# Kernel optimization log

Hardware: AMD Instinct MI355X
Metric: run time of the kernel (lower is better)

The kernel has to match this reference:

```python
import jax, jax.numpy as jnp
import numpy as np

D, DFF, H = 1024, 4096, 16
B, S, L = 4, 4096, 512


def setup_inputs() -> dict:
    key = jax.random.key(0)
    ks = jax.random.split(key, 16)
    w = lambda k, shape: (jax.random.normal(k, shape, jnp.float32) * 0.02)
    return {
        "x": jax.random.normal(ks[0], (B, S, D), jnp.float32),
        "limited_time_offer": jax.random.normal(ks[1], (B, L, D), jnp.float32),
        "src_src_self_mask": jnp.ones((B, 1, 1, S), bool),
        "lto_src_cross_mask": jnp.ones((B, 1, 1, S), bool),
        "sa_wq": w(ks[2], (D, D)), "sa_wk": w(ks[3], (D, D)),
        "sa_wv": w(ks[4], (D, D)), "sa_wo": w(ks[5], (D, D)),
        "ca_wq": w(ks[6], (D, D)), "ca_wk": w(ks[7], (D, D)),
        "ca_wv": w(ks[8], (D, D)), "ca_wo": w(ks[9], (D, D)),
        "ff_w1": w(ks[10], (D, DFF)), "ff_b1": jnp.zeros((DFF,), jnp.float32),
        "ff_w2": w(ks[11], (DFF, D)), "ff_b2": jnp.zeros((D,), jnp.float32),
        "ln1_a": jnp.ones((D,), jnp.float32), "ln1_b": jnp.zeros((D,), jnp.float32),
        "ln2_a": jnp.ones((D,), jnp.float32), "ln2_b": jnp.zeros((D,), jnp.float32),
        "ln3_a": jnp.ones((D,), jnp.float32), "ln3_b": jnp.zeros((D,), jnp.float32),
    }


def _ln(x, alpha, bias, eps=1e-6):
    # torch: (x - mean) / (std + eps), std is UNBIASED (ddof=1)
    mean = x.mean(axis=-1, keepdims=True)
    std = jnp.sqrt(x.var(axis=-1, ddof=1, keepdims=True))
    return alpha * (x - mean) / (std + eps) + bias


def _mha_linear(q_in, k_in, v_in, wq, wk, wv, wo):
    Bq, Nq, d = q_in.shape
    dk = d // H
    def proj(t, w):
        t = t @ w  # [b, n, d]
        return t.reshape(t.shape[0], t.shape[1], H, dk).transpose(0, 2, 1, 3)  # bhnd
    Q = jax.nn.relu(proj(q_in, wq)) + 1e-6
    K = jax.nn.relu(proj(k_in, wk)) + 1e-6
    V = proj(v_in, wv)
    kv = jnp.einsum('bhnd,bhne->bhde', K, V)          # KV outer-product state
    qk = jnp.einsum('bhnd,bhde->bhne', Q, kv)         # [b, h, nq, dk]
    # faithful to torch einsum('bhnd,bhne->bhn', Q, K.sum(2, keepdim)):
    # broadcasts n and sums d and e independently
    norm = 1.0 / (Q.sum(-1) * K.sum((2, 3))[:, :, None] + 1e-6)  # [b, h, nq]
    out = (qk * norm[..., None]).transpose(0, 2, 1, 3).reshape(Bq, Nq, d)
    return out @ wo


def reference(x, limited_time_offer, src_src_self_mask, lto_src_cross_mask,
              sa_wq, sa_wk, sa_wv, sa_wo,
              ca_wq, ca_wk, ca_wv, ca_wo,
              ff_w1, ff_b1, ff_w2, ff_b2,
              ln1_a, ln1_b, ln2_a, ln2_b, ln3_a, ln3_b):
    # residual 0: self attention on x
    xn = _ln(x, ln1_a, ln1_b)
    x = x + _mha_linear(xn, xn, xn, sa_wq, sa_wk, sa_wv, sa_wo)
    # residual 1: cross attention, queries = normed lto, keys/values = updated x
    lton = _ln(limited_time_offer, ln2_a, ln2_b)
    lto = limited_time_offer + _mha_linear(lton, x, x, ca_wq, ca_wk, ca_wv, ca_wo)
    # residual 2: feed forward
    fn = _ln(lto, ln3_a, ln3_b)
    ff = jax.nn.relu(fn @ ff_w1 + ff_b1) @ ff_w2 + ff_b2
    return lto + ff
```

## Files before the change

kernel.cpp:

```cpp
#include <hip/hip_runtime.h>
#include <hip/hip_bf16.h>

#define BATCH 4
#define SEQ   4096
#define LSEQ  512
#define DMODEL 1024
#define DFF_  4096
#define NHEAD 16
#define DK_   64
#define NSPLIT 8
#define FFSK  8

typedef __attribute__((ext_vector_type(4))) float f32x4;
typedef __attribute__((ext_vector_type(8))) __bf16 bf16x8;
typedef __attribute__((ext_vector_type(8))) unsigned short ushort8v;
typedef unsigned short u16;

__device__ __forceinline__ u16 f2bf(float f) {
  union { float f; unsigned int u; } c; c.f = f;
  unsigned int u = c.u;
  u += 0x7fffu + ((u >> 16) & 1u);
  return (u16)(u >> 16);
}
__device__ __forceinline__ float bf2f(u16 h) {
  union { unsigned int u; float f; } c; c.u = ((unsigned int)h) << 16;
  return c.f;
}
__device__ __forceinline__ void gload16(const void* g, void* l) {
  __builtin_amdgcn_global_load_lds(
      (const __attribute__((address_space(1))) unsigned int*)g,
      (__attribute__((address_space(3))) unsigned int*)l, 16, 0, 0);
}

__global__ __launch_bounds__(256) void ln_kernel(
    const float* __restrict__ x, const float* __restrict__ alpha,
    const float* __restrict__ beta, u16* __restrict__ y)
{
  const int row = blockIdx.x;
  const int t = threadIdx.x;
  const float4 v = ((const float4*)(x + (size_t)row * DMODEL))[t];
  float s = v.x + v.y + v.z + v.w;
  float ss = v.x * v.x + v.y * v.y + v.z * v.z + v.w * v.w;
  for (int off = 32; off >= 1; off >>= 1) {
    s += __shfl_xor(s, off);
    ss += __shfl_xor(ss, off);
  }
  __shared__ float sbuf[4], ssbuf[4];
  int w = t >> 6;
  if ((t & 63) == 0) { sbuf[w] = s; ssbuf[w] = ss; }
  __syncthreads();
  s = sbuf[0] + sbuf[1] + sbuf[2] + sbuf[3];
  ss = ssbuf[0] + ssbuf[1] + ssbuf[2] + ssbuf[3];
  float mean = s * (1.f / DMODEL);
  float var = (ss - mean * mean * DMODEL) * (1.f / (DMODEL - 1));
  var = fmaxf(var, 0.f);
  float inv = 1.f / (sqrtf(var) + 1e-6f);
  const float4 a = ((const float4*)alpha)[t];
  const float4 bb = ((const float4*)beta)[t];
  ushort4 o;
  o.x = f2bf(a.x * (v.x - mean) * inv + bb.x);
  o.y = f2bf(a.y * (v.y - mean) * inv + bb.y);
  o.z = f2bf(a.z * (v.z - mean) * inv + bb.z);
  o.w = f2bf(a.w * (v.w - mean) * inv + bb.w);
  ((ushort4*)(y + (size_t)row * DMODEL))[t] = o;
}

__global__ __launch_bounds__(256) void wconv_t_kernel(
    const float* __restrict__ W, u16* __restrict__ Wt, int K, int N)
{
  __shared__ float tile[32][33];
  const int n0 = blockIdx.x * 32, k0 = blockIdx.y * 32;
  const int t = threadIdx.x;
  const int r = t >> 3, c4 = (t & 7) * 4;
  float4 v = *(const float4*)&W[(size_t)(k0 + r) * N + n0 + c4];
  tile[r][c4 + 0] = v.x; tile[r][c4 + 1] = v.y;
  tile[r][c4 + 2] = v.z; tile[r][c4 + 3] = v.w;
  __syncthreads();
  ushort4 o;
  o.x = f2bf(tile[c4 + 0][r]);
  o.y = f2bf(tile[c4 + 1][r]);
  o.z = f2bf(tile[c4 + 2][r]);
  o.w = f2bf(tile[c4 + 3][r]);
  *(ushort4*)&Wt[(size_t)(n0 + r) * K + k0 + c4] = o;
}

template <int ACT, bool BIAS, bool RESID, bool OUTBF, bool SPLITK>
__global__ __launch_bounds__(512, 2) void gemm256(
    const u16* __restrict__ A, const u16* __restrict__ Bt,
    const float* __restrict__ bias, const float* __restrict__ R,
    void* __restrict__ Cout, int M, int N, int K, int lda, int ldb)
{
  __shared__ u16 sh[2][2][256 * 64];
  const int t = threadIdx.x;
  const int wid = t >> 6, lane = t & 63;
  const int wr = wid >> 2, wc = wid & 3;
  const int fr = lane & 15, fg = lane >> 4;

  if (SPLITK) {
    const int kp = blockIdx.y;
    A += (size_t)kp * K;
    Bt += (size_t)kp * K;
  }

  int bid = blockIdx.x;
  {
    const int nwg = gridDim.x;
    int q = nwg >> 3, rmd = nwg & 7;
    int xcd = bid & 7, idx = bid >> 3;
    bid = (xcd < rmd ? xcd * (q + 1) : rmd * (q + 1) + (xcd - rmd) * q) + idx;
  }
  const int nxb = N >> 8;
  const int m0 = (bid / nxb) * 256, n0 = (bid % nxb) * 256;

  auto stageA = [&](int buf, int h, int kt) {
#pragma unroll
    for (int j = 0; j < 2; ++j) {
      int idx = j * 512 + t;
      int r = idx >> 3;
      int gc = ((idx & 7) * 16) ^ ((r & 7) << 4);
      const char* src = (const char*)(A + (size_t)(m0 + h * 128 + r) * lda + kt * 64) + gc;
      char* dst = (char*)&sh[buf][0][0] + h * 16384 + j * 8192 + wid * 1024;
      gload16(src, dst);
    }
  };
  auto stageB = [&](int buf, int h, int kt) {
#pragma unroll
    for (int j = 0; j < 2; ++j) {
      int idx = j * 512 + t;
      int r = idx >> 3;
      int gc = ((idx & 7) * 16) ^ ((r & 7) << 4);
      const char* src = (const char*)(Bt + (size_t)(n0 + h * 128 + r) * ldb + kt * 64) + gc;
      char* dst = (char*)&sh[buf][1][0] + h * 16384 + j * 8192 + wid * 1024;
      gload16(src, dst);
    }
  };
  auto rdA = [&](int buf, int mi, int kk) -> bf16x8 {
    int r = wr * 128 + mi * 16 + fr;
    int c = (kk * 64 + fg * 16) ^ ((r & 7) << 4);
    return *(const bf16x8*)((const char*)&sh[buf][0][0] + r * 128 + c);
  };
  auto rdB = [&](int buf, int ni, int kk) -> bf16x8 {
    int r = wc * 64 + ni * 16 + fr;
    int c = (kk * 64 + fg * 16) ^ ((r & 7) << 4);
    return *(const bf16x8*)((const char*)&sh[buf][1][0] + r * 128 + c);
  };

  f32x4 acc[8][4] = {};
  bf16x8 bfrag[4][2];

#define PHASE(BUF, Q, STAGE_STMT, VCNT) do {                                          \
    bf16x8 a00 = rdA(BUF, (Q)*2, 0),     a01 = rdA(BUF, (Q)*2, 1);                     \
    bf16x8 a10 = rdA(BUF, (Q)*2 + 1, 0), a11 = rdA(BUF, (Q)*2 + 1, 1);                 \
    if ((Q) == 0) {                                                                    \
      _Pragma("unroll") for (int ni = 0; ni < 4; ++ni) {                               \
        bfrag[ni][0] = rdB(BUF, ni, 0); bfrag[ni][1] = rdB(BUF, ni, 1); } }            \
    STAGE_STMT;                                                                        \
    __builtin_amdgcn_s_barrier();                                                      \
    asm volatile("s_waitcnt lgkmcnt(0)" ::: "memory");                                 \
    __builtin_amdgcn_s_setprio(1);                                                     \
    _Pragma("unroll") for (int ni = 0; ni < 4; ++ni) {                                 \
      acc[(Q)*2][ni]     = __builtin_amdgcn_mfma_f32_16x16x32_bf16(a00, bfrag[ni][0], acc[(Q)*2][ni], 0, 0, 0);     \
      acc[(Q)*2][ni]     = __builtin_amdgcn_mfma_f32_16x16x32_bf16(a01, bfrag[ni][1], acc[(Q)*2][ni], 0, 0, 0);     \
      acc[(Q)*2 + 1][ni] = __builtin_amdgcn_mfma_f32_16x16x32_bf16(a10, bfrag[ni][0], acc[(Q)*2 + 1][ni], 0, 0, 0); \
      acc[(Q)*2 + 1][ni] = __builtin_amdgcn_mfma_f32_16x16x32_bf16(a11, bfrag[ni][1], acc[(Q)*2 + 1][ni], 0, 0, 0); } \
    __builtin_amdgcn_s_setprio(0);                                                     \
    if ((VCNT) == 4) { asm volatile("s_waitcnt vmcnt(4)" ::: "memory"); }              \
    else if ((VCNT) == 0) { asm volatile("s_waitcnt vmcnt(0)" ::: "memory"); }         \
    __builtin_amdgcn_s_barrier();                                                      \
  } while (0)

  stageA(0, 0, 0); stageA(0, 1, 0);
  stageB(0, 0, 0); stageB(0, 1, 0);
  stageB(1, 0, 1); stageB(1, 1, 1);
  asm volatile("s_waitcnt vmcnt(4)" ::: "memory");
  __builtin_amdgcn_s_barrier();

  const int NIT = K >> 7;
  for (int i = 0; i < NIT - 1; ++i) {
    const int t1 = 2 * i + 1, s0 = 2 * i + 2, s1 = 2 * i + 3;
    PHASE(0, 0, stageA(1, 0, t1), -1);
    PHASE(0, 1, stageA(1, 1, t1), -1);
    PHASE(0, 2, stageB(0, 0, s0), -1);
    PHASE(0, 3, stageB(0, 1, s0), 4);
    PHASE(1, 0, stageA(0, 0, s0), -1);
    PHASE(1, 1, stageA(0, 1, s0), -1);
    PHASE(1, 2, stageB(1, 0, s1), -1);
    PHASE(1, 3, stageB(1, 1, s1), 4);
  }
  {
    const int t1 = 2 * (NIT - 1) + 1;
    PHASE(0, 0, stageA(1, 0, t1), -1);
    PHASE(0, 1, stageA(1, 1, t1), -1);
    PHASE(0, 2, ((void)0), -1);
    PHASE(0, 3, ((void)0), 0);
    PHASE(1, 0, ((void)0), -1);
    PHASE(1, 1, ((void)0), -1);
    PHASE(1, 2, ((void)0), -1);
    PHASE(1, 3, ((void)0), -1);
  }
#undef PHASE

  float* Cf = (float*)Cout;
  if (SPLITK) Cf += (size_t)blockIdx.y * M * N;
  u16* Cb = (u16*)Cout;
  const bool segRelu = (ACT == 3) ? ((n0 >> 10) != 1) : false;
#pragma unroll
  for (int mi = 0; mi < 8; ++mi)
#pragma unroll
    for (int ni = 0; ni < 4; ++ni)
#pragma unroll
      for (int r = 0; r < 4; ++r) {
        int row = m0 + wr * 128 + mi * 16 + fg * 4 + r;
        int col = n0 + wc * 64 + ni * 16 + fr;
        float v = acc[mi][ni][r];
        if (BIAS) v += bias[col];
        if (ACT == 1) v = fmaxf(v, 0.f);
        if (ACT == 2) v = fmaxf(v, 0.f) + 1e-6f;
        if (ACT == 3 && segRelu) v = fmaxf(v, 0.f) + 1e-6f;
        if (RESID) v += R[(size_t)row * N + col];
        if (OUTBF) Cb[(size_t)row * N + col] = f2bf(v);
        else       Cf[(size_t)row * N + col] = v;
      }
}

__global__ __launch_bounds__(256) void ffred_kernel(
    const float* __restrict__ part, const float* __restrict__ bias,
    const float* __restrict__ R, float* __restrict__ out)
{
  const int idx = blockIdx.x * 256 + threadIdx.x;
  const int c4 = idx & 255;
  float4 s = ((const float4*)R)[idx];
  const float4 bv = ((const float4*)bias)[c4];
  s.x += bv.x; s.y += bv.y; s.z += bv.z; s.w += bv.w;
#pragma unroll
  for (int p = 0; p < FFSK; ++p) {
    float4 v = ((const float4*)part)[(size_t)p * 524288 + idx];
    s.x += v.x; s.y += v.y; s.z += v.z; s.w += v.w;
  }
  ((float4*)out)[idx] = s;
}

__global__ __launch_bounds__(256) void ffred_h_kernel(
    const float* __restrict__ part, const float* __restrict__ bias,
    u16* __restrict__ outb)
{
  const size_t idx = (size_t)blockIdx.x * 256 + threadIdx.x;
  const int c4 = idx & 1023;
  const float4 bv = ((const float4*)bias)[c4];
  const float4 p0 = ((const float4*)part)[idx];
  const float4 p1 = ((const float4*)part)[idx + 2097152];
  ushort4 o;
  o.x = f2bf(fmaxf(p0.x + p1.x + bv.x, 0.f));
  o.y = f2bf(fmaxf(p0.y + p1.y + bv.y, 0.f));
  o.z = f2bf(fmaxf(p0.z + p1.z + bv.z, 0.f));
  o.w = f2bf(fmaxf(p0.w + p1.w + bv.w, 0.f));
  ((ushort4*)outb)[idx] = o;
}

template <int ACT, bool BIAS, bool RESID, bool OUTBF>
__global__ __launch_bounds__(256) void gemm_bf16(
    const u16* __restrict__ A, const u16* __restrict__ Bt,
    const float* __restrict__ bias, const float* __restrict__ R,
    void* __restrict__ Cout, int M, int N, int K)
{
  __shared__ u16 As[2][128 * 32];
  __shared__ u16 Bs[2][128 * 32];
  const int t = threadIdx.x;
  const int m0 = blockIdx.y * 128, n0 = blockIdx.x * 128;
  const int lane = t & 63, wid = t >> 6;
  const int wm = (wid >> 1) * 64, wn = (wid & 1) * 64;
  const int fr = lane & 15, fg = lane >> 4;

  const int srow = t >> 2;
  const int scol = (t & 3) * 8;
  const u16* aptr = A + (size_t)(m0 + srow) * K + scol;
  const u16* bptr = Bt + (size_t)(n0 + srow) * K + scol;
  const size_t rstep = (size_t)64 * K;

  f32x4 acc[4][4] = {};

  auto stage = [&](int c, int k0) {
    gload16(aptr + k0,         &As[c][wid * 512]);
    gload16(aptr + k0 + rstep, &As[c][2048 + wid * 512]);
    gload16(bptr + k0,         &Bs[c][wid * 512]);
    gload16(bptr + k0 + rstep, &Bs[c][2048 + wid * 512]);
  };
  auto compute = [&](int c) {
    bf16x8 af[4], bfr[4];
#pragma unroll
    for (int mi = 0; mi < 4; ++mi)
      af[mi] = *(const bf16x8*)&As[c][(wm + mi * 16 + fr) * 32 + fg * 8];
#pragma unroll
    for (int ni = 0; ni < 4; ++ni)
      bfr[ni] = *(const bf16x8*)&Bs[c][(wn + ni * 16 + fr) * 32 + fg * 8];
#pragma unroll
    for (int mi = 0; mi < 4; ++mi)
#pragma unroll
      for (int ni = 0; ni < 4; ++ni)
        acc[mi][ni] = __builtin_amdgcn_mfma_f32_16x16x32_bf16(af[mi], bfr[ni], acc[mi][ni], 0, 0, 0);
  };

  const int NT = K >> 5;
  stage(0, 0);
  asm volatile("s_waitcnt vmcnt(0)" ::: "memory");
  __builtin_amdgcn_s_barrier();
  int cur = 0;
  for (int kt = 0; kt < NT - 1; ++kt) {
    stage(cur ^ 1, (kt + 1) * 32);
    compute(cur);
    asm volatile("s_waitcnt vmcnt(0)" ::: "memory");
    __builtin_amdgcn_s_barrier();
    cur ^= 1;
  }
  compute(cur);

  float* Cf = (float*)Cout;
  u16* Cb = (u16*)Cout;
#pragma unroll
  for (int mi = 0; mi < 4; ++mi)
#pragma unroll
    for (int ni = 0; ni < 4; ++ni)
#pragma unroll
      for (int r = 0; r < 4; ++r) {
        int row = m0 + wm + mi * 16 + fg * 4 + r;
        int col = n0 + wn + ni * 16 + fr;
        float v = acc[mi][ni][r];
        if (BIAS) v += bias[col];
        if (ACT == 1) v = fmaxf(v, 0.f);
        if (ACT == 2) v = fmaxf(v, 0.f) + 1e-6f;
        if (RESID) v += R[(size_t)row * N + col];
        if (OUTBF) Cb[(size_t)row * N + col] = f2bf(v);
        else       Cf[(size_t)row * N + col] = v;
      }
}

__global__ __launch_bounds__(256) void kv_mfma_kernel(
    const u16* __restrict__ KV, float* __restrict__ kvpart,
    float* __restrict__ kpart, int Ntok, int ld)
{
  const int h = blockIdx.x, b = blockIdx.y, sp = blockIdx.z;
  const int rows = Ntok / NSPLIT;
  const int nbeg = sp * rows;
  const u16* Kb = KV + ((size_t)b * Ntok + nbeg) * ld + h * DK_;
  const u16* Vb = Kb + 1024;
  __shared__ u16 Kt[64 * 64];
  __shared__ u16 Vt[64 * 64];
  const int t = threadIdx.x;
  const int lane = t & 63, wid = t >> 6;
  const int fr = lane & 15, fg = lane >> 4;
  const int lrow = t >> 2;
  const int lc0 = (t & 3) * 16;

  f32x4 acc[4] = {};
  float kp = 0.f;

  ushort8v ck[2], cv[2];
  {
    const u16* kr = Kb + (size_t)lrow * ld + lc0;
    const u16* vr = Vb + (size_t)lrow * ld + lc0;
    ck[0] = *(const ushort8v*)kr; ck[1] = *(const ushort8v*)(kr + 8);
    cv[0] = *(const ushort8v*)vr; cv[1] = *(const ushort8v*)(vr + 8);
  }
  for (int c = 0; c < rows; c += 64) {
#pragma unroll
    for (int i = 0; i < 2; ++i)
#pragma unroll
      for (int j = 0; j < 8; ++j) kp += bf2f(ck[i][j]);
    __syncthreads();
#pragma unroll
    for (int i = 0; i < 2; ++i)
#pragma unroll
      for (int j = 0; j < 8; ++j) {
        int d = lc0 + i * 8 + j;
        int byteoff = (d * 128 + lrow * 2) ^ ((d & 7) << 4);
        *(u16*)((char*)Kt + byteoff) = ck[i][j];
        *(u16*)((char*)Vt + byteoff) = cv[i][j];
      }
    __syncthreads();
    if (c + 64 < rows) {
      const u16* kr = Kb + (size_t)(c + 64 + lrow) * ld + lc0;
      const u16* vr = Vb + (size_t)(c + 64 + lrow) * ld + lc0;
      ck[0] = *(const ushort8v*)kr; ck[1] = *(const ushort8v*)(kr + 8);
      cv[0] = *(const ushort8v*)vr; cv[1] = *(const ushort8v*)(vr + 8);
    }
#pragma unroll
    for (int ks = 0; ks < 2; ++ks) {
      bf16x8 bv;
      {
        int e = wid * 16 + fr;
        int byteoff = (e * 128 + (ks * 32 + fg * 8) * 2) ^ ((e & 7) << 4);
        bv = *(const bf16x8*)((const char*)Vt + byteoff);
      }
#pragma unroll
      for (int mi = 0; mi < 4; ++mi) {
        int d = mi * 16 + fr;
        int byteoff = (d * 128 + (ks * 32 + fg * 8) * 2) ^ ((d & 7) << 4);
        bf16x8 av = *(const bf16x8*)((const char*)Kt + byteoff);
        acc[mi] = __builtin_amdgcn_mfma_f32_16x16x32_bf16(av, bv, acc[mi], 0, 0, 0);
      }
    }
  }
  float* outp = kvpart + (((size_t)(b * NHEAD + h)) * NSPLIT + sp) * (DK_ * DK_);
#pragma unroll
  for (int mi = 0; mi < 4; ++mi)
#pragma unroll
    for (int r = 0; r < 4; ++r)
      outp[(mi * 16 + fg * 4 + r) * DK_ + wid * 16 + fr] = acc[mi][r];
  for (int off = 32; off >= 1; off >>= 1) kp += __shfl_xor(kp, off);
  __shared__ float kr4[4];
  if (lane == 0) kr4[wid] = kp;
  __syncthreads();
  if (t == 0) kpart[(b * NHEAD + h) * NSPLIT + sp] = kr4[0] + kr4[1] + kr4[2] + kr4[3];
}

__global__ __launch_bounds__(256) void kv_reduce_kernel(
    const float* __restrict__ kvpart, const float* __restrict__ kpart,
    u16* __restrict__ kvT, float* __restrict__ ksum)
{
  const int bh = blockIdx.x;
  const int t = threadIdx.x;
  for (int i = t; i < DK_ * DK_; i += 256) {
    int d = i >> 6, e = i & 63;
    float s = 0.f;
#pragma unroll
    for (int p = 0; p < NSPLIT; ++p)
      s += kvpart[((size_t)bh * NSPLIT + p) * (DK_ * DK_) + i];
    kvT[(size_t)bh * (DK_ * DK_) + e * DK_ + d] = f2bf(s);
  }
  if (t == 0) {
    float s = 0.f;
    for (int p = 0; p < NSPLIT; ++p) s += kpart[bh * NSPLIT + p];
    ksum[bh] = s;
  }
}

__global__ __launch_bounds__(256) void qk_mfma_kernel(
    const u16* __restrict__ Qp, const u16* __restrict__ kvT,
    const float* __restrict__ ksum, u16* __restrict__ AO, int Ntok, int ldq)
{
  const int h = blockIdx.y, b = blockIdx.z;
  const int n0 = blockIdx.x * 128;
  const int t = threadIdx.x;
  const int lane = t & 63, wid = t >> 6;
  const int fr = lane & 15, fg = lane >> 4;

  __shared__ u16 Qs[128 * 64];
  __shared__ u16 KVs[64 * 64];
  __shared__ float qsl[128];

  auto swz = [](int byte, int row) { return byte ^ ((row & 7) << 4); };

  const u16* Qbase = Qp + ((size_t)b * Ntok + n0) * ldq + h * DK_;
#pragma unroll
  for (int j = 0; j < 4; ++j) {
    int id = t + 256 * j;
    int r = id >> 3, cseg = id & 7;
    ushort8v v = *(const ushort8v*)(Qbase + (size_t)r * ldq + cseg * 8);
    *(ushort8v*)((char*)Qs + swz(r * 128 + cseg * 16, r)) = v;
  }
  const u16* Kbase = kvT + ((size_t)(b * NHEAD + h)) * (DK_ * DK_);
#pragma unroll
  for (int j = 0; j < 2; ++j) {
    int id = t + 256 * j;
    int r = id >> 3, cseg = id & 7;
    ushort8v v = *(const ushort8v*)(Kbase + r * DK_ + cseg * 8);
    *(ushort8v*)((char*)KVs + swz(r * 128 + cseg * 16, r)) = v;
  }
  __syncthreads();

  {
    int row = t >> 1, part = t & 1;
    float s = 0.f;
#pragma unroll
    for (int j = 0; j < 4; ++j) {
      bf16x8 v = *(const bf16x8*)((char*)Qs + swz(row * 128 + (part * 4 + j) * 16, row));
#pragma unroll
      for (int i = 0; i < 8; ++i) s += (float)v[i];
    }
    s += __shfl_xor(s, 1);
    if (part == 0) qsl[row] = s;
  }

  const int wm = wid * 32;
  f32x4 acc[2][4] = {};
#pragma unroll
  for (int kk = 0; kk < 2; ++kk) {
    bf16x8 af[2], bfv[4];
#pragma unroll
    for (int mi = 0; mi < 2; ++mi) {
      int row = wm + mi * 16 + fr;
      af[mi] = *(const bf16x8*)((char*)Qs + swz(row * 128 + kk * 64 + fg * 16, row));
    }
#pragma unroll
    for (int ni = 0; ni < 4; ++ni) {
      int row = ni * 16 + fr;
      bfv[ni] = *(const bf16x8*)((char*)KVs + swz(row * 128 + kk * 64 + fg * 16, row));
    }
#pragma unroll
    for (int mi = 0; mi < 2; ++mi)
#pragma unroll
      for (int ni = 0; ni < 4; ++ni)
        acc[mi][ni] = __builtin_amdgcn_mfma_f32_16x16x32_bf16(af[mi], bfv[ni], acc[mi][ni], 0, 0, 0);
  }
  __syncthreads();

  const float ks = ksum[b * NHEAD + h];
  u16* AObase = AO + ((size_t)b * Ntok + n0) * DMODEL + h * DK_;
#pragma unroll
  for (int mi = 0; mi < 2; ++mi)
#pragma unroll
    for (int ni = 0; ni < 4; ++ni)
#pragma unroll
      for (int r = 0; r < 4; ++r) {
        int row = wm + mi * 16 + fg * 4 + r;
        int col = ni * 16 + fr;
        float rn = 1.f / (qsl[row] * ks + 1e-6f);
        AObase[(size_t)row * DMODEL + col] = f2bf(acc[mi][ni][r] * rn);
      }
}

extern "C" void kernel_launch(void* const* d_in, const int* in_sizes, int n_in,
                              void* d_out, int out_size, void* d_ws, size_t ws_size,
                              hipStream_t stream) {
  const float* x     = (const float*)d_in[0];
  const float* lto   = (const float*)d_in[1];
  const float* sa_wq = (const float*)d_in[4];
  const float* sa_wk = (const float*)d_in[5];
  const float* sa_wv = (const float*)d_in[6];
  const float* sa_wo = (const float*)d_in[7];
  const float* ca_wq = (const float*)d_in[8];
  const float* ca_wk = (const float*)d_in[9];
  const float* ca_wv = (const float*)d_in[10];
  const float* ca_wo = (const float*)d_in[11];
  const float* ff_w1 = (const float*)d_in[12];
  const float* ff_b1 = (const float*)d_in[13];
  const float* ff_w2 = (const float*)d_in[14];
  const float* ff_b2 = (const float*)d_in[15];
  const float* ln1_a = (const float*)d_in[16];
  const float* ln1_b = (const float*)d_in[17];
  const float* ln2_a = (const float*)d_in[18];
  const float* ln2_b = (const float*)d_in[19];
  const float* ln3_a = (const float*)d_in[20];
  const float* ln3_b = (const float*)d_in[21];
  float* out = (float*)d_out;

  char* wsb = (char*)d_ws;
  auto take = [&](size_t bytes) {
    char* p = wsb;
    wsb += (bytes + 255) & ~(size_t)255;
    return (void*)p;
  };
  u16* WKVQ = (u16*)take(6291456);
  u16* WCKV = (u16*)take(4194304);
  u16* SAOT = (u16*)take(2097152);
  u16* CQT  = (u16*)take(2097152);
  u16* COT  = (u16*)take(2097152);
  u16* FW1T = (u16*)take(8388608);
  u16* FW2T = (u16*)take(8388608);
  u16* R1   = (u16*)take(33554432);
  u16* KVQ  = (u16*)take(100663296);
  u16* R3   = (u16*)take(33554432);
  u16* S1 = (u16*)take(4194304);
  u16* S2 = (u16*)take(4194304);
  u16* S3 = (u16*)take(4194304);
  float* LTO1   = (float*)take(8388608);
  float* KVPART = (float*)take(8388608);
  u16*   KVT    = (u16*)take(1048576);
  float* KPART  = (float*)take(2048);
  float* KSUM   = (float*)take(256);
  float* FFPART = (float*)KVQ;

  const int STOK = BATCH * SEQ;
  const int LTOK = BATCH * LSEQ;
  dim3 blk(256);
  dim3 blk512(512);

  wconv_t_kernel<<<dim3(32, 32), blk, 0, stream>>>(sa_wk, WKVQ,           1024, 1024);
  wconv_t_kernel<<<dim3(32, 32), blk, 0, stream>>>(sa_wv, WKVQ + 1048576, 1024, 1024);
  wconv_t_kernel<<<dim3(32, 32), blk, 0, stream>>>(sa_wq, WKVQ + 2097152, 1024, 1024);
  wconv_t_kernel<<<dim3(32, 32), blk, 0, stream>>>(ca_wk, WCKV,           1024, 1024);
  wconv_t_kernel<<<dim3(32, 32), blk, 0, stream>>>(ca_wv, WCKV + 1048576, 1024, 1024);
  wconv_t_kernel<<<dim3(32, 32), blk, 0, stream>>>(sa_wo, SAOT, 1024, 1024);
  wconv_t_kernel<<<dim3(32, 32), blk, 0, stream>>>(ca_wq, CQT, 1024, 1024);
  wconv_t_kernel<<<dim3(32, 32), blk, 0, stream>>>(ca_wo, COT, 1024, 1024);
  wconv_t_kernel<<<dim3(128, 32), blk, 0, stream>>>(ff_w1, FW1T, 1024, 4096);
  wconv_t_kernel<<<dim3(32, 128), blk, 0, stream>>>(ff_w2, FW2T, 4096, 1024);

  ln_kernel<<<STOK, blk, 0, stream>>>(x, ln1_a, ln1_b, R1);
  gemm256<3, false, false, true, false><<<dim3(64 * 12), blk512, 0, stream>>>(
      R1, WKVQ, nullptr, nullptr, KVQ, STOK, 3072, 1024, 1024, 1024);
  kv_mfma_kernel<<<dim3(NHEAD, BATCH, NSPLIT), blk, 0, stream>>>(KVQ, KVPART, KPART, SEQ, 3072);
  kv_reduce_kernel<<<64, blk, 0, stream>>>(KVPART, KPART, KVT, KSUM);
  qk_mfma_kernel<<<dim3(SEQ / 128, NHEAD, BATCH), blk, 0, stream>>>(KVQ + 2048, KVT, KSUM, R1, SEQ, 3072);
  gemm256<0, false, true, true, false><<<dim3(64 * 4), blk512, 0, stream>>>(
      R1, SAOT, nullptr, x, R3, STOK, 1024, 1024, 1024, 1024);

  ln_kernel<<<LTOK, blk, 0, stream>>>(lto, ln2_a, ln2_b, S1);
  gemm_bf16<2, false, false, true><<<dim3(8, 16), blk, 0, stream>>>(S1, CQT, nullptr, nullptr, S2, LTOK, 1024, 1024);
  gemm256<3, false, false, true, false><<<dim3(64 * 8), blk512, 0, stream>>>(
      R3, WCKV, nullptr, nullptr, KVQ, STOK, 2048, 1024, 1024, 1024);
  kv_mfma_kernel<<<dim3(NHEAD, BATCH, NSPLIT), blk, 0, stream>>>(KVQ, KVPART, KPART, SEQ, 2048);
  kv_reduce_kernel<<<64, blk, 0, stream>>>(KVPART, KPART, KVT, KSUM);
  qk_mfma_kernel<<<dim3(LSEQ / 128, NHEAD, BATCH), blk, 0, stream>>>(S2, KVT, KSUM, S3, LSEQ, 1024);
  gemm_bf16<0, false, true, false><<<dim3(8, 16), blk, 0, stream>>>(S3, COT, nullptr, lto, LTO1, LTOK, 1024, 1024);

  ln_kernel<<<LTOK, blk, 0, stream>>>(LTO1, ln3_a, ln3_b, S1);
  gemm256<0, false, false, false, true><<<dim3(128, 2), blk512, 0, stream>>>(
      S1, FW1T, nullptr, nullptr, FFPART, LTOK, 4096, 512, 1024, 1024);
  ffred_h_kernel<<<8192, blk, 0, stream>>>(FFPART, ff_b1, R3);
  gemm256<0, false, false, false, true><<<dim3(32, FFSK), blk512, 0, stream>>>(
      R3, FW2T, nullptr, nullptr, FFPART, LTOK, 1024, 512, 4096, 4096);
  ffred_kernel<<<2048, blk, 0, stream>>>(FFPART, ff_b2, LTO1, out);
}
```

Baseline: 495.7 us.

## Batch weight conversions into one launch and restructure GEMM main-loop LDS pipelining

Merges the ten separate weight transpose/convert launches into a single 3D-grid launch, where the z index selects the weight matrix, to cut launch overhead. Also restructures the 256-tile GEMM inner loop. It now syncs once per buffer instead of twice per quarter-phase. It reloads B fragments per group and software-pipelines A fragment LDS reads one quarter ahead of the MFMAs. This reduces barrier count but raises register pressure, and correctness depends on the staging writes not overwriting the buffer being read.

```diff
diff --git a/kernel.cpp b/kernel.cpp
--- a/kernel.cpp
+++ b/kernel.cpp
@@ -65,11 +65,27 @@
   ((ushort4*)(y + (size_t)row * DMODEL))[t] = o;
 }
 
-__global__ __launch_bounds__(256) void wconv_t_kernel(
-    const float* __restrict__ W, u16* __restrict__ Wt, int K, int N)
-{
+__global__ __launch_bounds__(256) void wconv_all_kernel(
+    const float* w0, const float* w1, const float* w2, const float* w3,
+    const float* w4, const float* w5, const float* w6, const float* w7,
+    const float* w8, const float* w9,
+    u16* d0, u16* d1, u16* d2, u16* d3, u16* d4,
+    u16* d5, u16* d6, u16* d7, u16* d8, u16* d9)
+{
+  const int z = blockIdx.z;
+  const float* W; u16* Wt; int K, N;
+  int bx = blockIdx.x, by = blockIdx.y;
+  if (z < 8) {
+    const float* ws[8] = {w0, w1, w2, w3, w4, w5, w6, w7};
+    u16* ds[8] = {d0, d1, d2, d3, d4, d5, d6, d7};
+    W = ws[z]; Wt = ds[z]; K = 1024; N = 1024;
+  } else if (z < 12) {
+    W = w8; Wt = d8; K = 1024; N = 4096; bx += (z - 8) * 32;
+  } else {
+    W = w9; Wt = d9; K = 4096; N = 1024; by += (z - 12) * 32;
+  }
   __shared__ float tile[32][33];
-  const int n0 = blockIdx.x * 32, k0 = blockIdx.y * 32;
+  const int n0 = bx * 32, k0 = by * 32;
   const int t = threadIdx.x;
   const int r = t >> 3, c4 = (t & 7) * 4;
   float4 v = *(const float4*)&W[(size_t)(k0 + r) * N + n0 + c4];
@@ -146,27 +162,38 @@
   };
 
   f32x4 acc[8][4] = {};
-  bf16x8 bfrag[4][2];
-
-#define PHASE(BUF, Q, STAGE_STMT, VCNT) do {                                          \
-    bf16x8 a00 = rdA(BUF, (Q)*2, 0),     a01 = rdA(BUF, (Q)*2, 1);                     \
-    bf16x8 a10 = rdA(BUF, (Q)*2 + 1, 0), a11 = rdA(BUF, (Q)*2 + 1, 1);                 \
-    if ((Q) == 0) {                                                                    \
-      _Pragma("unroll") for (int ni = 0; ni < 4; ++ni) {                               \
-        bfrag[ni][0] = rdB(BUF, ni, 0); bfrag[ni][1] = rdB(BUF, ni, 1); } }            \
-    STAGE_STMT;                                                                        \
-    __builtin_amdgcn_s_barrier();                                                      \
-    asm volatile("s_waitcnt lgkmcnt(0)" ::: "memory");                                 \
-    __builtin_amdgcn_s_setprio(1);                                                     \
-    _Pragma("unroll") for (int ni = 0; ni < 4; ++ni) {                                 \
-      acc[(Q)*2][ni]     = __builtin_amdgcn_mfma_f32_16x16x32_bf16(a00, bfrag[ni][0], acc[(Q)*2][ni], 0, 0, 0);     \
-      acc[(Q)*2][ni]     = __builtin_amdgcn_mfma_f32_16x16x32_bf16(a01, bfrag[ni][1], acc[(Q)*2][ni], 0, 0, 0);     \
-      acc[(Q)*2 + 1][ni] = __builtin_amdgcn_mfma_f32_16x16x32_bf16(a10, bfrag[ni][0], acc[(Q)*2 + 1][ni], 0, 0, 0); \
-      acc[(Q)*2 + 1][ni] = __builtin_amdgcn_mfma_f32_16x16x32_bf16(a11, bfrag[ni][1], acc[(Q)*2 + 1][ni], 0, 0, 0); } \
-    __builtin_amdgcn_s_setprio(0);                                                     \
-    if ((VCNT) == 4) { asm volatile("s_waitcnt vmcnt(4)" ::: "memory"); }              \
-    else if ((VCNT) == 0) { asm volatile("s_waitcnt vmcnt(0)" ::: "memory"); }         \
-    __builtin_amdgcn_s_barrier();                                                      \
+
+#define MFMA_Q(Q, AF) do {                                                              \
+    __builtin_amdgcn_s_setprio(1);                                                      \
+    _Pragma("unroll") for (int ni = 0; ni < 4; ++ni) {                                  \
+      acc[(Q)*2][ni]     = __builtin_amdgcn_mfma_f32_16x16x32_bf16(AF[0], bfr[ni][0], acc[(Q)*2][ni], 0, 0, 0);     \
+      acc[(Q)*2][ni]     = __builtin_amdgcn_mfma_f32_16x16x32_bf16(AF[1], bfr[ni][1], acc[(Q)*2][ni], 0, 0, 0);     \
+      acc[(Q)*2 + 1][ni] = __builtin_amdgcn_mfma_f32_16x16x32_bf16(AF[2], bfr[ni][0], acc[(Q)*2 + 1][ni], 0, 0, 0); \
+      acc[(Q)*2 + 1][ni] = __builtin_amdgcn_mfma_f32_16x16x32_bf16(AF[3], bfr[ni][1], acc[(Q)*2 + 1][ni], 0, 0, 0); } \
+    __builtin_amdgcn_s_setprio(0);                                                      \
+  } while (0)
+
+#define GROUP(BUF, S1, S2, S3, S4, VC) do {                                             \
+    bf16x8 bfr[4][2];                                                                   \
+    _Pragma("unroll") for (int ni = 0; ni < 4; ++ni) {                                  \
+      bfr[ni][0] = rdB(BUF, ni, 0); bfr[ni][1] = rdB(BUF, ni, 1); }                     \
+    bf16x8 A0[4] = {rdA(BUF,0,0), rdA(BUF,0,1), rdA(BUF,1,0), rdA(BUF,1,1)};            \
+    asm volatile("s_waitcnt lgkmcnt(0)" ::: "memory");                                  \
+    __builtin_amdgcn_s_barrier();                                                       \
+    S1;                                                                                 \
+    bf16x8 A1[4] = {rdA(BUF,2,0), rdA(BUF,2,1), rdA(BUF,3,0), rdA(BUF,3,1)};            \
+    MFMA_Q(0, A0);                                                                      \
+    S2;                                                                                 \
+    bf16x8 A2[4] = {rdA(BUF,4,0), rdA(BUF,4,1), rdA(BUF,5,0), rdA(BUF,5,1)};            \
+    MFMA_Q(1, A1);                                                                      \
+    S3;                                                                                 \
+    bf16x8 A3[4] = {rdA(BUF,6,0), rdA(BUF,6,1), rdA(BUF,7,0), rdA(BUF,7,1)};            \
+    MFMA_Q(2, A2);                                                                      \
+    S4;                                                                                 \
+    MFMA_Q(3, A3);                                                                      \
+    if ((VC) == 4) { asm volatile("s_waitcnt vmcnt(4)" ::: "memory"); }                 \
+    else if ((VC) == 0) { asm volatile("s_waitcnt vmcnt(0)" ::: "memory"); }            \
+    __builtin_amdgcn_s_barrier();                                                       \
   } while (0)
 
   stageA(0, 0, 0); stageA(0, 1, 0);
@@ -178,27 +205,16 @@
   const int NIT = K >> 7;
   for (int i = 0; i < NIT - 1; ++i) {
     const int t1 = 2 * i + 1, s0 = 2 * i + 2, s1 = 2 * i + 3;
-    PHASE(0, 0, stageA(1, 0, t1), -1);
-    PHASE(0, 1, stageA(1, 1, t1), -1);
-    PHASE(0, 2, stageB(0, 0, s0), -1);
-    PHASE(0, 3, stageB(0, 1, s0), 4);
-    PHASE(1, 0, stageA(0, 0, s0), -1);
-    PHASE(1, 1, stageA(0, 1, s0), -1);
-    PHASE(1, 2, stageB(1, 0, s1), -1);
-    PHASE(1, 3, stageB(1, 1, s1), 4);
+    GROUP(0, stageA(1, 0, t1), stageA(1, 1, t1), stageB(0, 0, s0), stageB(0, 1, s0), 4);
+    GROUP(1, stageA(0, 0, s0), stageA(0, 1, s0), stageB(1, 0, s1), stageB(1, 1, s1), 4);
   }
   {
     const int t1 = 2 * (NIT - 1) + 1;
-    PHASE(0, 0, stageA(1, 0, t1), -1);
-    PHASE(0, 1, stageA(1, 1, t1), -1);
-    PHASE(0, 2, ((void)0), -1);
-    PHASE(0, 3, ((void)0), 0);
-    PHASE(1, 0, ((void)0), -1);
-    PHASE(1, 1, ((void)0), -1);
-    PHASE(1, 2, ((void)0), -1);
-    PHASE(1, 3, ((void)0), -1);
-  }
-#undef PHASE
+    GROUP(0, stageA(1, 0, t1), stageA(1, 1, t1), ((void)0), ((void)0), 0);
+    GROUP(1, ((void)0), ((void)0), ((void)0), ((void)0), -1);
+  }
+#undef GROUP
+#undef MFMA_Q
 
   float* Cf = (float*)Cout;
   if (SPLITK) Cf += (size_t)blockIdx.y * M * N;
@@ -575,16 +591,10 @@
   dim3 blk(256);
   dim3 blk512(512);
 
-  wconv_t_kernel<<<dim3(32, 32), blk, 0, stream>>>(sa_wk, WKVQ,           1024, 1024);
-  wconv_t_kernel<<<dim3(32, 32), blk, 0, stream>>>(sa_wv, WKVQ + 1048576, 1024, 1024);
-  wconv_t_kernel<<<dim3(32, 32), blk, 0, stream>>>(sa_wq, WKVQ + 2097152, 1024, 1024);
-  wconv_t_kernel<<<dim3(32, 32), blk, 0, stream>>>(ca_wk, WCKV,           1024, 1024);
-  wconv_t_kernel<<<dim3(32, 32), blk, 0, stream>>>(ca_wv, WCKV + 1048576, 1024, 1024);
-  wconv_t_kernel<<<dim3(32, 32), blk, 0, stream>>>(sa_wo, SAOT, 1024, 1024);
-  wconv_t_kernel<<<dim3(32, 32), blk, 0, stream>>>(ca_wq, CQT, 1024, 1024);
-  wconv_t_kernel<<<dim3(32, 32), blk, 0, stream>>>(ca_wo, COT, 1024, 1024);
-  wconv_t_kernel<<<dim3(128, 32), blk, 0, stream>>>(ff_w1, FW1T, 1024, 4096);
-  wconv_t_kernel<<<dim3(32, 128), blk, 0, stream>>>(ff_w2, FW2T, 4096, 1024);
+  wconv_all_kernel<<<dim3(32, 32, 16), blk, 0, stream>>>(
+      sa_wk, sa_wv, sa_wq, ca_wk, ca_wv, sa_wo, ca_wq, ca_wo, ff_w1, ff_w2,
+      WKVQ, WKVQ + 1048576, WKVQ + 2097152, WCKV, WCKV + 1048576,
+      SAOT, CQT, COT, FW1T, FW2T);
 
   ln_kernel<<<STOK, blk, 0, stream>>>(x, ln1_a, ln1_b, R1);
   gemm256<3, false, false, true, false><<<dim3(64 * 12), blk512, 0, stream>>>(
```

Result: no change. 489.5 us (-1.3%).
